# Kernel tuning notes

Measured on AMD Instinct MI355X. Metric: run time of the kernel, lower is better.

## Reference

```python
import jax, jax.numpy as jnp
import numpy as np
from jax import lax

B, C_IN, C_OUT, H, W, K, PAD = 4, 64, 64, 96, 96, 3, 1
K2 = K * K


def setup_inputs() -> dict:
    key = jax.random.key(0)
    k1, k2, k3, k4, k5 = jax.random.split(key, 5)
    x = jax.random.normal(k1, (B, C_IN, H, W), jnp.float32)
    offset = jax.random.normal(k2, (B, 2 * K2, H, W), jnp.float32)
    weight = jax.random.normal(k3, (C_OUT, C_IN, K, K), jnp.float32) * 0.05
    mask_weight = jax.random.normal(k4, (K2, C_IN, K, K), jnp.float32) * 0.05
    mask_bias = jax.random.normal(k5, (K2,), jnp.float32) * 0.05
    return {"x": x, "offset": offset, "weight": weight,
            "mask_weight": mask_weight, "mask_bias": mask_bias}


def _deform_conv2d(x, offset, weight, mask):
    # torchvision ordering: per kernel tap k, offset[:, 2k] is dy, offset[:, 2k+1] is dx
    off_y = offset[:, 0::2]  # [B, K2, H, W]
    off_x = offset[:, 1::2]
    ky, kx = jnp.meshgrid(jnp.arange(K), jnp.arange(K), indexing="ij")
    ky = ky.reshape(K2).astype(x.dtype)
    kx = kx.reshape(K2).astype(x.dtype)
    hh = jnp.arange(H, dtype=x.dtype)
    ww = jnp.arange(W, dtype=x.dtype)
    base_y = hh[None, :, None] - PAD + ky[:, None, None]   # [K2, H, 1]
    base_x = ww[None, None, :] - PAD + kx[:, None, None]   # [K2, 1, W]
    py = base_y[None] + off_y                               # [B, K2, H, W]
    px = base_x[None] + off_x

    y0 = jnp.floor(py)
    x0 = jnp.floor(px)
    wy = py - y0   # bilinear weights
    wx = px - x0
    y0i = y0.astype(jnp.int32)
    x0i = x0.astype(jnp.int32)

    x_flat = x.reshape(B, C_IN, H * W)

    def gather(yy, xx):
        valid = (yy >= 0) & (yy < H) & (xx >= 0) & (xx < W)
        idx = jnp.clip(yy, 0, H - 1) * W + jnp.clip(xx, 0, W - 1)  # [B,K2,H,W]
        idx_f = idx.reshape(B, -1)
        v = jax.vmap(lambda xf, i: xf[:, i])(x_flat, idx_f)  # [B, C, K2*H*W]
        v = v.reshape(B, C_IN, K2, H, W)
        return v * valid[:, None].astype(v.dtype)

    v00 = gather(y0i, x0i)
    v01 = gather(y0i, x0i + 1)
    v10 = gather(y0i + 1, x0i)
    v11 = gather(y0i + 1, x0i + 1)

    wy_ = wy[:, None]  # [B,1,K2,H,W]
    wx_ = wx[:, None]
    sampled = (v00 * (1 - wy_) * (1 - wx_) + v01 * (1 - wy_) * wx_
               + v10 * wy_ * (1 - wx_) + v11 * wy_ * wx_)
    sampled = sampled * mask[:, None]  # modulate by sigmoid mask

    w2 = weight.reshape(C_OUT, C_IN, K2)
    return jnp.einsum("bckhw,ock->bohw", sampled, w2)


def reference(x, offset, weight, mask_weight, mask_bias):
    mask_logits = lax.conv_general_dilated(
        x, mask_weight, window_strides=(1, 1), padding=[(PAD, PAD), (PAD, PAD)],
        dimension_numbers=("NCHW", "OIHW", "NCHW"))
    mask = jax.nn.sigmoid(mask_logits + mask_bias[None, :, None, None])
    return _deform_conv2d(x, offset, weight, mask)
```

## Files before the change

### kernel.cpp

```cpp
#include <hip/hip_runtime.h>
#include <math.h>

#define BB 4
#define CI 64
#define CO 64
#define HH 96
#define WW 96
#define HW (HH*WW)
#define K2 9
#define PADC 1

#define TW 4
#define TH 4
#define TPXT 16
#define TBX (WW/TW)
#define TBY (HH/TH)
#define NTILES (BB*TBX*TBY)
#define GRID 480

#define WC 16
#define SREC 70
#define RING 16
#define NSLOT (RING*WC)

typedef __attribute__((ext_vector_type(8))) short short8;
typedef __attribute__((ext_vector_type(4))) float float4v;

#define WF_USHORTS (18*64*32)
#define MWF_USHORTS (18*16*32)

__device__ __forceinline__ float bf2f(short s) {
    return __uint_as_float(((unsigned int)(unsigned short)s) << 16);
}
__device__ __forceinline__ short f2bf(float f) {
    unsigned int u = __float_as_uint(f);
    u = (u + 0x7fffu + ((u >> 16) & 1u)) >> 16;
    return (short)u;
}

__global__ __launch_bounds__(256) void pack_kernel(const float* __restrict__ wgt,
                                                   const float* __restrict__ mw,
                                                   unsigned short* __restrict__ Wf,
                                                   unsigned short* __restrict__ MWf) {
    int i = blockIdx.x * 256 + threadIdx.x;
    if (i < WF_USHORTS) {
        int frag = i >> 11;
        int o = (i >> 5) & 63;
        int tt = i & 31;
        int k = frag >> 1, cc = frag & 1;
        int c = cc * 32 + tt;
        Wf[i] = (unsigned short)f2bf(wgt[o * 576 + c * 9 + k]);
    } else if (i < WF_USHORTS + MWF_USHORTS) {
        int e = i - WF_USHORTS;
        int frag = e >> 9;
        int m = (e >> 5) & 15;
        int tt = e & 31;
        int q = frag >> 1, cc = frag & 1;
        int c = cc * 32 + tt;
        MWf[e] = (m < 9) ? (unsigned short)f2bf(mw[m * 576 + c * 9 + q]) : 0;
    }
}

struct SmemT {
    unsigned short win[NSLOT * SREC];
    float mred[2][2][K2][TPXT];
    int   idx[K2][4][TPXT];
    float w[K2][4][TPXT];
    float part[3][16][64];
};

__device__ __forceinline__ short8 ld_win(const unsigned int* w32, int dw) {
    union { unsigned int u[4]; short8 s; } z;
    z.u[0] = w32[dw + 0];
    z.u[1] = w32[dw + 1];
    z.u[2] = w32[dw + 2];
    z.u[3] = w32[dw + 3];
    return z.s;
}

__device__ __forceinline__ void stage_rows(unsigned int* w32, int t, int rs0, int nr,
                                           int wc0, const float* __restrict__ xb) {
    int ntask = nr * 128;
    for (int e = t; e < ntask; e += 256) {
        int ri = e >> 7;
        int chp = (e >> 2) & 31;
        int c4 = e & 3;
        int label = rs0 + ri;
        int row = min(max(label, 0), HH - 1);
        int rslot = (label & 15) * WC;
        int c0c = wc0 + c4 * 4;
        const float* s0 = xb + (size_t)(2 * chp) * HW + row * WW;
        const float* s1 = s0 + HW;
        float v0[4], v1[4];
        if (c0c >= 0 && c0c + 3 < WW) {
            float4v a = *(const float4v*)(s0 + c0c);
            float4v bq = *(const float4v*)(s1 + c0c);
            v0[0]=a[0]; v0[1]=a[1]; v0[2]=a[2]; v0[3]=a[3];
            v1[0]=bq[0]; v1[1]=bq[1]; v1[2]=bq[2]; v1[3]=bq[3];
        } else {
            #pragma unroll
            for (int j = 0; j < 4; j++) {
                int cc2 = min(max(c0c + j, 0), WW - 1);
                v0[j] = s0[cc2]; v1[j] = s1[cc2];
            }
        }
        #pragma unroll
        for (int j = 0; j < 4; j++) {
            unsigned int pk = (unsigned short)f2bf(v0[j]) |
                              ((unsigned int)(unsigned short)f2bf(v1[j]) << 16);
            w32[(rslot + c4 * 4 + j) * 35 + chp] = pk;
        }
    }
}

template<int KB, int KE>
__device__ __forceinline__ void run_strip(SmemT& sm, int t, int wv, int ch, int tg,
                                          const float* __restrict__ x,
                                          const float* __restrict__ off,
                                          const float* __restrict__ mbias,
                                          const unsigned short* __restrict__ Wf,
                                          const unsigned short* __restrict__ MWf,
                                          float* __restrict__ out, int bid) {
    constexpr int NK = KE - KB;
    int lane = t & 63;
    int n = lane & 15, quad = lane >> 4;
    unsigned int* w32 = (unsigned int*)sm.win;
    const unsigned int* w32c = (const unsigned int*)sm.win;

    int g = bid & 7, r = bid >> 3;
    int b = g & 3, txh = g >> 2;
    int col = r / 5, s = r % 5;
    int tx = txh * 12 + col;
    int ty0 = (s < 4) ? s * 5 : 20;
    int len = (s < 4) ? 5 : 4;
    int w0 = tx * TW;
    int wc0 = w0 - 4;
    const float* xb = x + (size_t)b * CI * HW;

    short8 wA[NK][4];
    short8 mA[NK];
    #pragma unroll
    for (int kk = 0; kk < NK; kk++) {
        int k = KB + kk;
        const unsigned short* wp = Wf + (size_t)((k * 2 + ch) * 64) * 32 + quad * 8;
        #pragma unroll
        for (int ss = 0; ss < 4; ss++)
            wA[kk][ss] = *(const short8*)(wp + (ss * 16 + n) * 32);
        mA[kk] = *(const short8*)(MWf + ((size_t)((k * 2 + ch) * 16 + n)) * 32 + quad * 8);
    }

    int ly = n >> 2, lx = n & 3;
    int cbase_dw = ch * 16 + quad * 4;

    for (int j = 0; j < len; j++) {
        int ty = ty0 + j;
        int h0 = ty * TH;
        int h = h0 + ly, wcc = w0 + lx;

        if (j == 0) stage_rows(w32, t, h0 - 4, 13, wc0, xb);
        else        stage_rows(w32, t, h0 + 5, 4, wc0, xb);
        __syncthreads();

        {
            float4v macc = {0.f, 0.f, 0.f, 0.f};
            #pragma unroll
            for (int kk = 0; kk < NK; kk++) {
                int q = KB + kk;
                int hh = h + q / 3 - 1, ww2 = wcc + q % 3 - 1;
                bool valid = (hh >= 0) && (hh < HH) && (ww2 >= 0) && (ww2 < WW);
                short8 bfrag = {0, 0, 0, 0, 0, 0, 0, 0};
                if (valid) {
                    int slot = (hh & 15) * WC + (ww2 - wc0);
                    bfrag = ld_win(w32c, slot * 35 + cbase_dw);
                }
                macc = __builtin_amdgcn_mfma_f32_16x16x32_bf16(mA[kk], bfrag, macc, 0, 0, 0);
            }
            #pragma unroll
            for (int rr = 0; rr < 4; rr++) {
                int row = quad * 4 + rr;
                if (row < 9) sm.mred[ch][tg][row][n] = macc[rr];
            }
        }
        __syncthreads();

        if (t < K2 * TPXT) {
            int k = t >> 4, pe = t & 15;
            int ph = h0 + (pe >> 2), pw = w0 + (pe & 3);
            int p = ph * WW + pw;
            float oy = off[((size_t)b * 2 * K2 + 2 * k) * HW + p];
            float ox = off[((size_t)b * 2 * K2 + 2 * k + 1) * HW + p];
            float sl = sm.mred[0][0][k][pe] + sm.mred[0][1][k][pe] +
                       sm.mred[1][0][k][pe] + sm.mred[1][1][k][pe] + mbias[k];
            float m = 1.f / (1.f + expf(-sl));
            float py  = (float)(ph - PADC + k / 3) + oy;
            float pxf = (float)(pw - PADC + k % 3) + ox;
            float y0f = floorf(py), x0f = floorf(pxf);
            float wy = py - y0f, wx = pxf - x0f;
            int y0 = (int)y0f, x0 = (int)x0f;
            int y1 = y0 + 1, x1 = x0 + 1;
            int y0c = min(max(y0, 0), HH - 1), y1c = min(max(y1, 0), HH - 1);
            int x0c = min(max(x0, 0), WW - 1), x1c = min(max(x1, 0), WW - 1);
            bool vy0 = (y0 >= 0) && (y0 < HH), vy1 = (y1 >= 0) && (y1 < HH);
            bool vx0 = (x0 >= 0) && (x0 < WW), vx1 = (x1 >= 0) && (x1 < WW);
            float w00 = (1.f - wy) * (1.f - wx) * m; if (!(vy0 && vx0)) w00 = 0.f;
            float w01 = (1.f - wy) * wx * m;         if (!(vy0 && vx1)) w01 = 0.f;
            float w10 = wy * (1.f - wx) * m;         if (!(vy1 && vx0)) w10 = 0.f;
            float w11 = wy * wx * m;                 if (!(vy1 && vx1)) w11 = 0.f;
            sm.idx[k][0][pe] = (y0c << 16) | x0c;
            sm.idx[k][1][pe] = (y0c << 16) | x1c;
            sm.idx[k][2][pe] = (y1c << 16) | x0c;
            sm.idx[k][3][pe] = (y1c << 16) | x1c;
            sm.w[k][0][pe] = w00; sm.w[k][1][pe] = w01;
            sm.w[k][2][pe] = w10; sm.w[k][3][pe] = w11;
        }
        __syncthreads();

        float4v acc0 = {0.f, 0.f, 0.f, 0.f};
        float4v acc1 = {0.f, 0.f, 0.f, 0.f};
        float4v acc2 = {0.f, 0.f, 0.f, 0.f};
        float4v acc3 = {0.f, 0.f, 0.f, 0.f};
        const float* xfb = xb + (size_t)(ch * 32 + quad * 8) * HW;

        #pragma unroll
        for (int kk = 0; kk < NK; kk++) {
            int k = KB + kk;
            short8 U[4];
            #pragma unroll
            for (int cor = 0; cor < 4; cor++) {
                int yx = sm.idx[k][cor][n];
                int yy = yx >> 16, xx = yx & 0xffff;
                bool inw = (yy >= h0 - 4) && (yy <= h0 + 8) &&
                           (xx >= wc0) && (xx <= wc0 + 15);
                short8 u;
                if (inw) {
                    int slot = (yy & 15) * WC + (xx - wc0);
                    u = ld_win(w32c, slot * 35 + cbase_dw);
                } else {
                    const float* fs = xfb + yy * WW + xx;
                    #pragma unroll
                    for (int jj = 0; jj < 8; jj++) u[jj] = f2bf(fs[(size_t)jj * HW]);
                }
                U[cor] = u;
            }
            float w0v = sm.w[k][0][n], w1v = sm.w[k][1][n];
            float w2v = sm.w[k][2][n], w3v = sm.w[k][3][n];
            short8 bfrag;
            #pragma unroll
            for (int jj = 0; jj < 8; jj++) {
                float v = bf2f(U[0][jj]) * w0v + bf2f(U[1][jj]) * w1v +
                          bf2f(U[2][jj]) * w2v + bf2f(U[3][jj]) * w3v;
                bfrag[jj] = f2bf(v);
            }
            acc0 = __builtin_amdgcn_mfma_f32_16x16x32_bf16(wA[kk][0], bfrag, acc0, 0, 0, 0);
            acc1 = __builtin_amdgcn_mfma_f32_16x16x32_bf16(wA[kk][1], bfrag, acc1, 0, 0, 0);
            acc2 = __builtin_amdgcn_mfma_f32_16x16x32_bf16(wA[kk][2], bfrag, acc2, 0, 0, 0);
            acc3 = __builtin_amdgcn_mfma_f32_16x16x32_bf16(wA[kk][3], bfrag, acc3, 0, 0, 0);
        }

        if (wv != 0) {
            #pragma unroll
            for (int rr = 0; rr < 4; rr++) {
                sm.part[wv - 1][0 * 4 + rr][lane] = acc0[rr];
                sm.part[wv - 1][1 * 4 + rr][lane] = acc1[rr];
                sm.part[wv - 1][2 * 4 + rr][lane] = acc2[rr];
                sm.part[wv - 1][3 * 4 + rr][lane] = acc3[rr];
            }
        }
        __syncthreads();
        if (wv == 0) {
            float* ob = out + (size_t)b * CO * HW + h * WW + wcc;
            #pragma unroll
            for (int rr = 0; rr < 4; rr++) {
                int j0 = rr, j1 = 4 + rr, j2 = 8 + rr, j3 = 12 + rr;
                ob[(size_t)(0 * 16 + quad * 4 + rr) * HW] = acc0[rr] +
                    sm.part[0][j0][lane] + sm.part[1][j0][lane] + sm.part[2][j0][lane];
                ob[(size_t)(1 * 16 + quad * 4 + rr) * HW] = acc1[rr] +
                    sm.part[0][j1][lane] + sm.part[1][j1][lane] + sm.part[2][j1][lane];
                ob[(size_t)(2 * 16 + quad * 4 + rr) * HW] = acc2[rr] +
                    sm.part[0][j2][lane] + sm.part[1][j2][lane] + sm.part[2][j2][lane];
                ob[(size_t)(3 * 16 + quad * 4 + rr) * HW] = acc3[rr] +
                    sm.part[0][j3][lane] + sm.part[1][j3][lane] + sm.part[2][j3][lane];
            }
        }
        __syncthreads();
    }
}

__global__ __launch_bounds__(256, 2) void fused_kernel(const float* __restrict__ x,
                                                       const float* __restrict__ off,
                                                       const float* __restrict__ mbias,
                                                       const unsigned short* __restrict__ Wf,
                                                       const unsigned short* __restrict__ MWf,
                                                       float* __restrict__ out) {
    __shared__ SmemT sm;
    int t = threadIdx.x;
    int wv = t >> 6;
    int ch = wv & 1, tg = wv >> 1;
    if (tg == 0)
        run_strip<0, 5>(sm, t, wv, ch, tg, x, off, mbias, Wf, MWf, out, blockIdx.x);
    else
        run_strip<5, 9>(sm, t, wv, ch, tg, x, off, mbias, Wf, MWf, out, blockIdx.x);
}

extern "C" void kernel_launch(void* const* d_in, const int* in_sizes, int n_in,
                              void* d_out, int out_size, void* d_ws, size_t ws_size,
                              hipStream_t stream) {
    const float* x   = (const float*)d_in[0];
    const float* off = (const float*)d_in[1];
    const float* wgt = (const float*)d_in[2];
    const float* mw  = (const float*)d_in[3];
    const float* mb  = (const float*)d_in[4];
    float* out = (float*)d_out;

    unsigned short* Wf  = (unsigned short*)d_ws;
    unsigned short* MWf = Wf + WF_USHORTS;

    hipLaunchKernelGGL(pack_kernel, dim3((WF_USHORTS + MWF_USHORTS + 255) / 256), dim3(256),
                       0, stream, wgt, mw, Wf, MWf);
    hipLaunchKernelGGL(fused_kernel, dim3(GRID), dim3(256), 0, stream,
                       x, off, mb, Wf, MWf, out);
}
```

Baseline: 106.8 us.

## Prefetch next strip rows and offsets into registers, shorten strips, raise occupancy

Each block now handles a fixed 3-tile strip, so the grid grows to 768 blocks, and launch bounds rise to 3 blocks per CU. The global loads for the next tile's window rows and offsets are issued before the current tile's compute and written to shared memory afterwards, which hides load latency behind MFMA work. The cross-wave reduction becomes a two-level tree using a smaller shared buffer. bf16 packing switches to the hardware float2-to-bfloat162 intrinsic with packed dword arithmetic. The risks are register pressure from holding the prefetched rows at the higher occupancy target, and more redundant halo staging because strips are shorter.

```diff
diff --git a/kernel.cpp b/kernel.cpp
--- a/kernel.cpp
+++ b/kernel.cpp
@@ -1,4 +1,5 @@
 #include <hip/hip_runtime.h>
+#include <hip/hip_bf16.h>
 #include <math.h>
 
 #define BB 4
@@ -15,27 +16,30 @@
 #define TPXT 16
 #define TBX (WW/TW)
 #define TBY (HH/TH)
-#define NTILES (BB*TBX*TBY)
-#define GRID 480
+#define SLEN 3
+#define GRID 768
 
 #define WC 16
 #define SREC 70
-#define RING 16
-#define NSLOT (RING*WC)
+#define NSLOT (16*WC)
 
 typedef __attribute__((ext_vector_type(8))) short short8;
 typedef __attribute__((ext_vector_type(4))) float float4v;
+typedef __attribute__((ext_vector_type(4))) unsigned int uint4v;
 
 #define WF_USHORTS (18*64*32)
 #define MWF_USHORTS (18*16*32)
 
-__device__ __forceinline__ float bf2f(short s) {
-    return __uint_as_float(((unsigned int)(unsigned short)s) << 16);
-}
 __device__ __forceinline__ short f2bf(float f) {
     unsigned int u = __float_as_uint(f);
     u = (u + 0x7fffu + ((u >> 16) & 1u)) >> 16;
     return (short)u;
+}
+__device__ __forceinline__ unsigned int pkbf(float lo, float hi) {
+    float2 f; f.x = lo; f.y = hi;
+    union { __hip_bfloat162 h; unsigned int u; } z;
+    z.h = __float22bfloat162_rn(f);
+    return z.u;
 }
 
 __global__ __launch_bounds__(256) void pack_kernel(const float* __restrict__ wgt,
@@ -66,51 +70,43 @@
     float mred[2][2][K2][TPXT];
     int   idx[K2][4][TPXT];
     float w[K2][4][TPXT];
-    float part[3][16][64];
+    float part[2][16][64];
 };
 
-__device__ __forceinline__ short8 ld_win(const unsigned int* w32, int dw) {
-    union { unsigned int u[4]; short8 s; } z;
-    z.u[0] = w32[dw + 0];
-    z.u[1] = w32[dw + 1];
-    z.u[2] = w32[dw + 2];
-    z.u[3] = w32[dw + 3];
+__device__ __forceinline__ uint4v ld_win4(const unsigned int* w32, int dw) {
+    uint4v z;
+    z[0] = w32[dw + 0]; z[1] = w32[dw + 1];
+    z[2] = w32[dw + 2]; z[3] = w32[dw + 3];
+    return z;
+}
+__device__ __forceinline__ short8 ld_win8(const unsigned int* w32, int dw) {
+    union { uint4v u; short8 s; } z;
+    z.u = ld_win4(w32, dw);
     return z.s;
 }
 
-__device__ __forceinline__ void stage_rows(unsigned int* w32, int t, int rs0, int nr,
-                                           int wc0, const float* __restrict__ xb) {
-    int ntask = nr * 128;
-    for (int e = t; e < ntask; e += 256) {
-        int ri = e >> 7;
-        int chp = (e >> 2) & 31;
-        int c4 = e & 3;
-        int label = rs0 + ri;
-        int row = min(max(label, 0), HH - 1);
-        int rslot = (label & 15) * WC;
-        int c0c = wc0 + c4 * 4;
-        const float* s0 = xb + (size_t)(2 * chp) * HW + row * WW;
-        const float* s1 = s0 + HW;
-        float v0[4], v1[4];
-        if (c0c >= 0 && c0c + 3 < WW) {
-            float4v a = *(const float4v*)(s0 + c0c);
-            float4v bq = *(const float4v*)(s1 + c0c);
-            v0[0]=a[0]; v0[1]=a[1]; v0[2]=a[2]; v0[3]=a[3];
-            v1[0]=bq[0]; v1[1]=bq[1]; v1[2]=bq[2]; v1[3]=bq[3];
-        } else {
-            #pragma unroll
-            for (int j = 0; j < 4; j++) {
-                int cc2 = min(max(c0c + j, 0), WW - 1);
-                v0[j] = s0[cc2]; v1[j] = s1[cc2];
-            }
-        }
+__device__ __forceinline__ void stage_load(const float* __restrict__ xb, int label,
+                                           int chp, int c0c, float4v* a, float4v* bq) {
+    int row = min(max(label, 0), HH - 1);
+    const float* s0 = xb + (size_t)(2 * chp) * HW + row * WW;
+    const float* s1 = s0 + HW;
+    if (c0c >= 0 && c0c + 3 < WW) {
+        *a = *(const float4v*)(s0 + c0c);
+        *bq = *(const float4v*)(s1 + c0c);
+    } else {
         #pragma unroll
         for (int j = 0; j < 4; j++) {
-            unsigned int pk = (unsigned short)f2bf(v0[j]) |
-                              ((unsigned int)(unsigned short)f2bf(v1[j]) << 16);
-            w32[(rslot + c4 * 4 + j) * 35 + chp] = pk;
-        }
-    }
+            int cc2 = min(max(c0c + j, 0), WW - 1);
+            (*a)[j] = s0[cc2]; (*bq)[j] = s1[cc2];
+        }
+    }
+}
+__device__ __forceinline__ void stage_write(unsigned int* w32, int label, int chp,
+                                            int c4, float4v a, float4v bq) {
+    int rslot = (label & 15) * WC;
+    #pragma unroll
+    for (int j = 0; j < 4; j++)
+        w32[(rslot + c4 * 4 + j) * 35 + chp] = pkbf(a[j], bq[j]);
 }
 
 template<int KB, int KE>
@@ -129,10 +125,9 @@
 
     int g = bid & 7, r = bid >> 3;
     int b = g & 3, txh = g >> 2;
-    int col = r / 5, s = r % 5;
+    int col = r >> 3, s = r & 7;
     int tx = txh * 12 + col;
-    int ty0 = (s < 4) ? s * 5 : 20;
-    int len = (s < 4) ? 5 : 4;
+    int ty0 = s * SLEN;
     int w0 = tx * TW;
     int wc0 = w0 - 4;
     const float* xb = x + (size_t)b * CI * HW;
@@ -152,14 +147,43 @@
     int ly = n >> 2, lx = n & 3;
     int cbase_dw = ch * 16 + quad * 4;
 
-    for (int j = 0; j < len; j++) {
-        int ty = ty0 + j;
-        int h0 = ty * TH;
+    for (int e = t; e < 13 * 128; e += 256) {
+        int ri = e >> 7, chp = (e >> 2) & 31, c4 = e & 3;
+        float4v a, bq;
+        stage_load(xb, ty0 * TH - 4 + ri, chp, wc0 + c4 * 4, &a, &bq);
+        stage_write(w32, ty0 * TH - 4 + ri, chp, c4, a, bq);
+    }
+    bool bm = t < K2 * TPXT;
+    int km = t >> 4, pem = t & 15;
+    float mbr = 0.f;
+    size_t offy_base = ((size_t)b * 2 * K2 + 2 * km) * HW;
+    size_t offx_base = offy_base + HW;
+    float poy = 0.f, pox = 0.f;
+    if (bm) {
+        mbr = mbias[km];
+        int p = (ty0 * TH + (pem >> 2)) * WW + w0 + (pem & 3);
+        poy = off[offy_base + p];
+        pox = off[offx_base + p];
+    }
+
+    for (int j = 0; j < SLEN; j++) {
+        int h0 = (ty0 + j) * TH;
         int h = h0 + ly, wcc = w0 + lx;
-
-        if (j == 0) stage_rows(w32, t, h0 - 4, 13, wc0, xb);
-        else        stage_rows(w32, t, h0 + 5, 4, wc0, xb);
-        __syncthreads();
+        __syncthreads();
+
+        float4v pa0, pb0, pa1, pb1;
+        float noy = 0.f, nox = 0.f;
+        bool hn = (j + 1 < SLEN);
+        if (hn) {
+            int e1 = t + 256;
+            stage_load(xb, h0 + 9 + (t >> 7), (t >> 2) & 31, wc0 + (t & 3) * 4, &pa0, &pb0);
+            stage_load(xb, h0 + 9 + (e1 >> 7), (e1 >> 2) & 31, wc0 + (e1 & 3) * 4, &pa1, &pb1);
+            if (bm) {
+                int p = (h0 + 4 + (pem >> 2)) * WW + w0 + (pem & 3);
+                noy = off[offy_base + p];
+                nox = off[offx_base + p];
+            }
+        }
 
         {
             float4v macc = {0.f, 0.f, 0.f, 0.f};
@@ -171,7 +195,7 @@
                 short8 bfrag = {0, 0, 0, 0, 0, 0, 0, 0};
                 if (valid) {
                     int slot = (hh & 15) * WC + (ww2 - wc0);
-                    bfrag = ld_win(w32c, slot * 35 + cbase_dw);
+                    bfrag = ld_win8(w32c, slot * 35 + cbase_dw);
                 }
                 macc = __builtin_amdgcn_mfma_f32_16x16x32_bf16(mA[kk], bfrag, macc, 0, 0, 0);
             }
@@ -183,17 +207,13 @@
         }
         __syncthreads();
 
-        if (t < K2 * TPXT) {
-            int k = t >> 4, pe = t & 15;
-            int ph = h0 + (pe >> 2), pw = w0 + (pe & 3);
-            int p = ph * WW + pw;
-            float oy = off[((size_t)b * 2 * K2 + 2 * k) * HW + p];
-            float ox = off[((size_t)b * 2 * K2 + 2 * k + 1) * HW + p];
-            float sl = sm.mred[0][0][k][pe] + sm.mred[0][1][k][pe] +
-                       sm.mred[1][0][k][pe] + sm.mred[1][1][k][pe] + mbias[k];
+        if (bm) {
+            int ph = h0 + (pem >> 2), pw = w0 + (pem & 3);
+            float sl = sm.mred[0][0][km][pem] + sm.mred[0][1][km][pem] +
+                       sm.mred[1][0][km][pem] + sm.mred[1][1][km][pem] + mbr;
             float m = 1.f / (1.f + expf(-sl));
-            float py  = (float)(ph - PADC + k / 3) + oy;
-            float pxf = (float)(pw - PADC + k % 3) + ox;
+            float py  = (float)(ph - PADC + km / 3) + poy;
+            float pxf = (float)(pw - PADC + km % 3) + pox;
             float y0f = floorf(py), x0f = floorf(pxf);
             float wy = py - y0f, wx = pxf - x0f;
             int y0 = (int)y0f, x0 = (int)x0f;
@@ -206,12 +226,12 @@
             float w01 = (1.f - wy) * wx * m;         if (!(vy0 && vx1)) w01 = 0.f;
             float w10 = wy * (1.f - wx) * m;         if (!(vy1 && vx0)) w10 = 0.f;
             float w11 = wy * wx * m;                 if (!(vy1 && vx1)) w11 = 0.f;
-            sm.idx[k][0][pe] = (y0c << 16) | x0c;
-            sm.idx[k][1][pe] = (y0c << 16) | x1c;
-            sm.idx[k][2][pe] = (y1c << 16) | x0c;
-            sm.idx[k][3][pe] = (y1c << 16) | x1c;
-            sm.w[k][0][pe] = w00; sm.w[k][1][pe] = w01;
-            sm.w[k][2][pe] = w10; sm.w[k][3][pe] = w11;
+            sm.idx[km][0][pem] = (y0c << 16) | x0c;
+            sm.idx[km][1][pem] = (y0c << 16) | x1c;
+            sm.idx[km][2][pem] = (y1c << 16) | x0c;
+            sm.idx[km][3][pem] = (y1c << 16) | x1c;
+            sm.w[km][0][pem] = w00; sm.w[km][1][pem] = w01;
+            sm.w[km][2][pem] = w10; sm.w[km][3][pem] = w11;
         }
         __syncthreads();
 
@@ -224,46 +244,79 @@
         #pragma unroll
         for (int kk = 0; kk < NK; kk++) {
             int k = KB + kk;
-            short8 U[4];
+            uint4v U[4];
             #pragma unroll
             for (int cor = 0; cor < 4; cor++) {
                 int yx = sm.idx[k][cor][n];
                 int yy = yx >> 16, xx = yx & 0xffff;
                 bool inw = (yy >= h0 - 4) && (yy <= h0 + 8) &&
                            (xx >= wc0) && (xx <= wc0 + 15);
-                short8 u;
+                uint4v u;
                 if (inw) {
                     int slot = (yy & 15) * WC + (xx - wc0);
-                    u = ld_win(w32c, slot * 35 + cbase_dw);
+                    u = ld_win4(w32c, slot * 35 + cbase_dw);
                 } else {
                     const float* fs = xfb + yy * WW + xx;
                     #pragma unroll
-                    for (int jj = 0; jj < 8; jj++) u[jj] = f2bf(fs[(size_t)jj * HW]);
+                    for (int dd = 0; dd < 4; dd++)
+                        u[dd] = pkbf(fs[(size_t)(2 * dd) * HW], fs[(size_t)(2 * dd + 1) * HW]);
                 }
                 U[cor] = u;
             }
             float w0v = sm.w[k][0][n], w1v = sm.w[k][1][n];
             float w2v = sm.w[k][2][n], w3v = sm.w[k][3][n];
-            short8 bfrag;
-            #pragma unroll
-            for (int jj = 0; jj < 8; jj++) {
-                float v = bf2f(U[0][jj]) * w0v + bf2f(U[1][jj]) * w1v +
-                          bf2f(U[2][jj]) * w2v + bf2f(U[3][jj]) * w3v;
-                bfrag[jj] = f2bf(v);
-            }
-            acc0 = __builtin_amdgcn_mfma_f32_16x16x32_bf16(wA[kk][0], bfrag, acc0, 0, 0, 0);
-            acc1 = __builtin_amdgcn_mfma_f32_16x16x32_bf16(wA[kk][1], bfrag, acc1, 0, 0, 0);
-            acc2 = __builtin_amdgcn_mfma_f32_16x16x32_bf16(wA[kk][2], bfrag, acc2, 0, 0, 0);
-            acc3 = __builtin_amdgcn_mfma_f32_16x16x32_bf16(wA[kk][3], bfrag, acc3, 0, 0, 0);
-        }
-
-        if (wv != 0) {
-            #pragma unroll
-            for (int rr = 0; rr < 4; rr++) {
-                sm.part[wv - 1][0 * 4 + rr][lane] = acc0[rr];
-                sm.part[wv - 1][1 * 4 + rr][lane] = acc1[rr];
-                sm.part[wv - 1][2 * 4 + rr][lane] = acc2[rr];
-                sm.part[wv - 1][3 * 4 + rr][lane] = acc3[rr];
+            union { unsigned int u[4]; short8 s; } bf;
+            #pragma unroll
+            for (int dd = 0; dd < 4; dd++) {
+                float lo = __uint_as_float(U[0][dd] << 16) * w0v
+                         + __uint_as_float(U[1][dd] << 16) * w1v
+                         + __uint_as_float(U[2][dd] << 16) * w2v
+                         + __uint_as_float(U[3][dd] << 16) * w3v;
+                float hi = __uint_as_float(U[0][dd] & 0xffff0000u) * w0v
+                         + __uint_as_float(U[1][dd] & 0xffff0000u) * w1v
+                         + __uint_as_float(U[2][dd] & 0xffff0000u) * w2v
+                         + __uint_as_float(U[3][dd] & 0xffff0000u) * w3v;
+                bf.u[dd] = pkbf(lo, hi);
+            }
+            acc0 = __builtin_amdgcn_mfma_f32_16x16x32_bf16(wA[kk][0], bf.s, acc0, 0, 0, 0);
+            acc1 = __builtin_amdgcn_mfma_f32_16x16x32_bf16(wA[kk][1], bf.s, acc1, 0, 0, 0);
+            acc2 = __builtin_amdgcn_mfma_f32_16x16x32_bf16(wA[kk][2], bf.s, acc2, 0, 0, 0);
+            acc3 = __builtin_amdgcn_mfma_f32_16x16x32_bf16(wA[kk][3], bf.s, acc3, 0, 0, 0);
+        }
+
+        if (wv >= 2) {
+            #pragma unroll
+            for (int rr = 0; rr < 4; rr++) {
+                sm.part[wv - 2][0 * 4 + rr][lane] = acc0[rr];
+                sm.part[wv - 2][1 * 4 + rr][lane] = acc1[rr];
+                sm.part[wv - 2][2 * 4 + rr][lane] = acc2[rr];
+                sm.part[wv - 2][3 * 4 + rr][lane] = acc3[rr];
+            }
+        }
+        __syncthreads();
+        if (wv == 1) {
+            #pragma unroll
+            for (int rr = 0; rr < 4; rr++) {
+                acc0[rr] += sm.part[1][0 * 4 + rr][lane];
+                acc1[rr] += sm.part[1][1 * 4 + rr][lane];
+                acc2[rr] += sm.part[1][2 * 4 + rr][lane];
+                acc3[rr] += sm.part[1][3 * 4 + rr][lane];
+            }
+            #pragma unroll
+            for (int rr = 0; rr < 4; rr++) {
+                sm.part[1][0 * 4 + rr][lane] = acc0[rr];
+                sm.part[1][1 * 4 + rr][lane] = acc1[rr];
+                sm.part[1][2 * 4 + rr][lane] = acc2[rr];
+                sm.part[1][3 * 4 + rr][lane] = acc3[rr];
+            }
+        }
+        if (wv == 0) {
+            #pragma unroll
+            for (int rr = 0; rr < 4; rr++) {
+                acc0[rr] += sm.part[0][0 * 4 + rr][lane];
+                acc1[rr] += sm.part[0][1 * 4 + rr][lane];
+                acc2[rr] += sm.part[0][2 * 4 + rr][lane];
+                acc3[rr] += sm.part[0][3 * 4 + rr][lane];
             }
         }
         __syncthreads();
@@ -271,22 +324,23 @@
             float* ob = out + (size_t)b * CO * HW + h * WW + wcc;
             #pragma unroll
             for (int rr = 0; rr < 4; rr++) {
-                int j0 = rr, j1 = 4 + rr, j2 = 8 + rr, j3 = 12 + rr;
-                ob[(size_t)(0 * 16 + quad * 4 + rr) * HW] = acc0[rr] +
-                    sm.part[0][j0][lane] + sm.part[1][j0][lane] + sm.part[2][j0][lane];
-                ob[(size_t)(1 * 16 + quad * 4 + rr) * HW] = acc1[rr] +
-                    sm.part[0][j1][lane] + sm.part[1][j1][lane] + sm.part[2][j1][lane];
-                ob[(size_t)(2 * 16 + quad * 4 + rr) * HW] = acc2[rr] +
-                    sm.part[0][j2][lane] + sm.part[1][j2][lane] + sm.part[2][j2][lane];
-                ob[(size_t)(3 * 16 + quad * 4 + rr) * HW] = acc3[rr] +
-                    sm.part[0][j3][lane] + sm.part[1][j3][lane] + sm.part[2][j3][lane];
-            }
-        }
-        __syncthreads();
-    }
-}
-
-__global__ __launch_bounds__(256, 2) void fused_kernel(const float* __restrict__ x,
+                ob[(size_t)(0 * 16 + quad * 4 + rr) * HW] = acc0[rr] + sm.part[1][0 * 4 + rr][lane];
+                ob[(size_t)(1 * 16 + quad * 4 + rr) * HW] = acc1[rr] + sm.part[1][1 * 4 + rr][lane];
+                ob[(size_t)(2 * 16 + quad * 4 + rr) * HW] = acc2[rr] + sm.part[1][2 * 4 + rr][lane];
+                ob[(size_t)(3 * 16 + quad * 4 + rr) * HW] = acc3[rr] + sm.part[1][3 * 4 + rr][lane];
+            }
+        }
+
+        if (hn) {
+            int e1 = t + 256;
+            stage_write(w32, h0 + 9 + (t >> 7), (t >> 2) & 31, t & 3, pa0, pb0);
+            stage_write(w32, h0 + 9 + (e1 >> 7), (e1 >> 2) & 31, e1 & 3, pa1, pb1);
+            poy = noy; pox = nox;
+        }
+    }
+}
+
+__global__ __launch_bounds__(256, 3) void fused_kernel(const float* __restrict__ x,
                                                        const float* __restrict__ off,
                                                        const float* __restrict__ mbias,
                                                        const unsigned short* __restrict__ Wf,
```

Measured after the change: 108.1 us. No clear change (+1.2%).
